# Kernel optimization log

Measured on AMD Instinct MI355X. Metric: run time of the kernel, lower is better.

The kernel has to match this reference:

```python
import jax, jax.numpy as jnp
import numpy as np

NUM_HEADS = 16
NUM_GROUPS = 4
HIDDEN = 2048
HEAD_DIM = HIDDEN // NUM_HEADS  # 128


def setup_inputs() -> dict:
    key = jax.random.key(0)
    ks = jax.random.split(key, 9)
    B, S = 2, 2048
    kv_dim = NUM_GROUPS * HEAD_DIM
    sc_in = 1.0 / np.sqrt(HIDDEN)
    return {
        "X": jax.random.normal(ks[0], (B, S, HIDDEN), dtype=jnp.float32),
        "Wq": jax.random.normal(ks[1], (HIDDEN, HIDDEN), dtype=jnp.float32) * sc_in,
        "bq": jnp.zeros((HIDDEN,), jnp.float32),
        "Wk": jax.random.normal(ks[2], (kv_dim, HIDDEN), dtype=jnp.float32) * sc_in,
        "bk": jnp.zeros((kv_dim,), jnp.float32),
        "Wv": jax.random.normal(ks[3], (kv_dim, HIDDEN), dtype=jnp.float32) * sc_in,
        "bv": jnp.zeros((kv_dim,), jnp.float32),
        "Wo": jax.random.normal(ks[4], (HIDDEN, HIDDEN), dtype=jnp.float32) * sc_in,
        "bo": jnp.zeros((HIDDEN,), jnp.float32),
    }


def reference(X, Wq, bq, Wk, bk, Wv, bv, Wo, bo):
    B, S, D = X.shape
    H, G, hd = NUM_HEADS, NUM_GROUPS, HEAD_DIM
    rep = H // G

    q = X @ Wq.T + bq                          # (B,S,D)
    k = X @ Wk.T + bk                          # (B,S,G*hd)
    v = X @ Wv.T + bv                          # (B,S,G*hd)

    q = q.reshape(B, S, H, hd).transpose(0, 2, 1, 3)   # (B,H,S,hd)
    k = k.reshape(B, S, G, hd).transpose(0, 2, 1, 3)   # (B,G,S,hd)
    v = v.reshape(B, S, G, hd).transpose(0, 2, 1, 3)
    # GQA head expansion: each kv group serves rep query heads
    k = jnp.repeat(k, rep, axis=1)             # (B,H,S,hd)
    v = jnp.repeat(v, rep, axis=1)

    scale = 1.0 / jnp.sqrt(jnp.asarray(hd, X.dtype))
    scores = jnp.einsum('bhqd,bhkd->bhqk', q, k) * scale  # (B,H,S,S)
    attn = jax.nn.softmax(scores, axis=-1)
    mid = jnp.einsum('bhqk,bhkd->bhqd', attn, v)          # (B,H,S,hd)
    mid = mid.transpose(0, 2, 1, 3).reshape(B, S, D)
    return mid @ Wo.T + bo
```

## Files before the change

kernel.cpp:

```cpp
#include <hip/hip_runtime.h>

using uint = unsigned int;
using ushort = unsigned short;

typedef float f32x4 __attribute__((ext_vector_type(4)));
typedef float f32x16 __attribute__((ext_vector_type(16)));
typedef uint u32x4 __attribute__((ext_vector_type(4)));
using short8 = __attribute__((ext_vector_type(8))) short;

__device__ __forceinline__ ushort f2bf(float f) {
  uint u = __float_as_uint(f);
  u += 0x7fffu + ((u >> 16) & 1u);
  return (ushort)(u >> 16);
}

#define GLOAD_LDS16(gptr, lptr)                                                   \
  __builtin_amdgcn_global_load_lds(                                               \
      (const __attribute__((address_space(1))) void*)(gptr),                      \
      (__attribute__((address_space(3))) void*)(lptr), 16, 0, 0)

__global__ void cast_all_bf16(const float* __restrict__ X,
                              const float* __restrict__ Wq,
                              const float* __restrict__ Wk,
                              const float* __restrict__ Wv,
                              const float* __restrict__ Wo,
                              ushort* __restrict__ dst ) {
  const int e0 = 2097152;
  const int e1 = e0 + 1048576;
  const int e2 = e1 + 262144;
  const int e3 = e2 + 262144;
  const int e4 = e3 + 1048576;
  const int stride = gridDim.x * blockDim.x;
  for (int i = blockIdx.x * blockDim.x + threadIdx.x; i < e4; i += stride) {
    const float* src;
    int j;
    if (i < e0)      { src = X;  j = i; }
    else if (i < e1) { src = Wq; j = i - e0; }
    else if (i < e2) { src = Wk; j = i - e1; }
    else if (i < e3) { src = Wv; j = i - e2; }
    else             { src = Wo; j = i - e3; }
    float4 v = reinterpret_cast<const float4*>(src)[j];
    ushort4 o;
    o.x = f2bf(v.x); o.y = f2bf(v.y); o.z = f2bf(v.z); o.w = f2bf(v.w);
    reinterpret_cast<ushort4*>(dst)[i] = o;
  }
}

__device__ __forceinline__ void gemm128_mainloop(const ushort* __restrict__ A,
                                                 const ushort* __restrict__ W,
                                                 int K, ushort* As, ushort* Bs,
                                                 f32x4 (&acc)[4][4]) {
  const int tid = threadIdx.x;
  const int lane = tid & 63;
  const int wr = (tid >> 7) & 1;
  const int wc = (tid >> 6) & 1;
  const char* aP = (const char*)(A + (size_t)(tid >> 2) * K) + (tid & 3) * 16;
  const char* bP = (const char*)(W + (size_t)(tid >> 2) * K) + (tid & 3) * 16;
  const size_t rowHop = (size_t)64 * K * 2;
  ushort* aL0 = As + tid * 8;
  ushort* aL1 = As + 2048 + tid * 8;
  ushort* bL0 = Bs + tid * 8;
  ushort* bL1 = Bs + 2048 + tid * 8;
  const int ar = lane & 15;
  const int ak = (lane >> 4) * 8;

  for (int k0 = 0; k0 < K; k0 += 32) {
    GLOAD_LDS16(aP, aL0);
    GLOAD_LDS16(aP + rowHop, aL1);
    GLOAD_LDS16(bP, bL0);
    GLOAD_LDS16(bP + rowHop, bL1);
    aP += 64; bP += 64;
    __syncthreads();
    short8 af[4], bf[4];
#pragma unroll
    for (int i = 0; i < 4; ++i)
      af[i] = *reinterpret_cast<const short8*>(&As[(wr * 64 + i * 16 + ar) * 32 + ak]);
#pragma unroll
    for (int i = 0; i < 4; ++i)
      bf[i] = *reinterpret_cast<const short8*>(&Bs[(wc * 64 + i * 16 + ar) * 32 + ak]);
#pragma unroll
    for (int mi = 0; mi < 4; ++mi)
#pragma unroll
      for (int ni = 0; ni < 4; ++ni)
        acc[mi][ni] = __builtin_amdgcn_mfma_f32_16x16x32_bf16(af[mi], bf[ni],
                                                              acc[mi][ni], 0, 0, 0);
    __syncthreads();
  }
}

__global__ __launch_bounds__(256) void qkv_gemm(
    const ushort* __restrict__ Xb, const ushort* __restrict__ Wq,
    const ushort* __restrict__ Wk, const ushort* __restrict__ Wv,
    const float* __restrict__ bq, const float* __restrict__ bk,
    const float* __restrict__ bv, ushort* __restrict__ Qb,
    ushort* __restrict__ Kb, ushort* __restrict__ Vf) {
  __shared__ ushort As[128 * 32], Bs[128 * 32];
  const int bx = blockIdx.x, by = blockIdx.y;
  const ushort* W; const float* bias; ushort* out;
  int n0, mode, ldo;
  if (bx < 16)      { W = Wq; bias = bq; out = Qb; n0 = bx * 128;        mode = 0; ldo = 2048; }
  else if (bx < 20) { W = Wk; bias = bk; out = Kb; n0 = (bx - 16) * 128; mode = 0; ldo = 512; }
  else              { W = Wv; bias = bv; out = Vf; n0 = (bx - 20) * 128; mode = 1; ldo = 0; }

  f32x4 acc[4][4] = {};
  gemm128_mainloop(Xb + (size_t)by * 128 * 2048, W + (size_t)n0 * 2048, 2048, As, Bs, acc);

  const int lane = threadIdx.x & 63;
  const int wr = (threadIdx.x >> 7) & 1, wc = (threadIdx.x >> 6) & 1;
  const int r0 = by * 128 + wr * 64 + ((lane >> 4) * 4);
  const int c0 = wc * 64 + (lane & 15);
#pragma unroll
  for (int mi = 0; mi < 4; ++mi)
#pragma unroll
    for (int ni = 0; ni < 4; ++ni) {
      const int col = c0 + ni * 16;
      const float bb = bias[n0 + col];
#pragma unroll
      for (int j = 0; j < 4; ++j) {
        const int row = r0 + mi * 16 + j;
        const float v = acc[mi][ni][j] + bb;
        if (mode == 0) {
          out[(size_t)row * ldo + n0 + col] = f2bf(v);
        } else {
          const int b2 = row >> 11, s = row & 2047;
          const int vc = n0 + col;
          const int g2 = vc >> 7, d = vc & 127;
          const int t2 = s >> 6, ks = (s >> 4) & 3, hi2 = (s >> 3) & 1, j2 = s & 7;
          const int dblk = d >> 5, lq2 = d & 31;
          out[(size_t)((b2 * 4 + g2) * 32 + t2) * 8192 +
              (ks * 4 + dblk) * 512 + (hi2 * 32 + lq2) * 8 + j2] = f2bf(v);
        }
      }
    }
}

__global__ __launch_bounds__(256) void out_gemm(const ushort* __restrict__ Mid,
                                                const ushort* __restrict__ Wo,
                                                const float* __restrict__ bo,
                                                float* __restrict__ Out) {
  __shared__ ushort As[128 * 32], Bs[128 * 32];
  const int bx = blockIdx.x, by = blockIdx.y;
  f32x4 acc[4][4] = {};
  gemm128_mainloop(Mid + (size_t)by * 128 * 2048, Wo + (size_t)bx * 128 * 2048,
                   2048, As, Bs, acc);
  const int lane = threadIdx.x & 63;
  const int wr = (threadIdx.x >> 7) & 1, wc = (threadIdx.x >> 6) & 1;
  const int r0 = by * 128 + wr * 64 + ((lane >> 4) * 4);
  const int c0 = bx * 128 + wc * 64 + (lane & 15);
#pragma unroll
  for (int mi = 0; mi < 4; ++mi)
#pragma unroll
    for (int ni = 0; ni < 4; ++ni) {
      const int col = c0 + ni * 16;
      const float bb = bo[col];
#pragma unroll
      for (int j = 0; j < 4; ++j)
        Out[(size_t)(r0 + mi * 16 + j) * 2048 + col] = acc[mi][ni][j] + bb;
    }
}

__global__ __launch_bounds__(256, 2) void attn_fwd(const ushort* __restrict__ Q,
                                                   const ushort* __restrict__ Kb,
                                                   const ushort* __restrict__ Vf,
                                                   ushort* __restrict__ Mid) {
  __shared__ ushort Ks[2][64 * 128];

  const int tid = threadIdx.x, lane = tid & 63, wave = tid >> 6;
  const int h = blockIdx.y, b = blockIdx.z, g = h >> 2;
  const int q0w = blockIdx.x * 128 + wave * 32;
  const int lq = lane & 31, hi = lane >> 5;

  const char* kbase = (const char*)Kb + ((size_t)b * 2048 * 512 + g * 128) * 2;
  int kRow[4], kOff[4];
#pragma unroll
  for (int i = 0; i < 4; ++i) {
    const int off = (i * 256 + tid) * 16;
    const int r = off >> 8, c = off & 255;
    kRow[i] = r; kOff[i] = c ^ ((r & 15) << 4);
  }

#pragma unroll
  for (int i = 0; i < 4; ++i)
    GLOAD_LDS16(kbase + (size_t)kRow[i] * 1024 + kOff[i],
                (char*)Ks[0] + (i * 256 + tid) * 16);

  const ushort* vfb = Vf + (size_t)(b * 4 + g) * 262144 + lane * 8;

  short8 qf[8];
  {
    const ushort* qp = Q + (size_t)(b * 2048 + q0w + lq) * 2048 + h * 128 + hi * 8;
#pragma unroll
    for (int dblk = 0; dblk < 8; ++dblk)
      qf[dblk] = *reinterpret_cast<const short8*>(qp + dblk * 16);
  }

  short8 onesf;
#pragma unroll
  for (int i = 0; i < 8; ++i) onesf[i] = (short)0x3F80;

  f32x16 o[4] = {};
  f32x16 ol = {};
  const float sc2 = 0.08838834764831843f * 1.44269504088896340736f;
  const float FM = 8.0f;

  __syncthreads();

  const int ksw = (lq & 15) << 4;

  for (int t = 0; t < 32; ++t) {
    const int cur = t & 1;

    short8 vr[16];
    {
      const ushort* vt = vfb + t * 8192;
#pragma unroll
      for (int u = 0; u < 16; ++u)
        vr[u] = *reinterpret_cast<const short8*>(vt + u * 512);
    }

    if (t < 31) {
      const int kv0 = (t + 1) * 64;
#pragma unroll
      for (int i = 0; i < 4; ++i)
        GLOAD_LDS16(kbase + (size_t)(kv0 + kRow[i]) * 1024 + kOff[i],
                    (char*)Ks[cur ^ 1] + (i * 256 + tid) * 16);
    }

    const char* ksb = (const char*)Ks[cur];
    f32x16 st0 = {}, st1 = {};
    __builtin_amdgcn_s_setprio(1);
#pragma unroll
    for (int dblk = 0; dblk < 8; ++dblk) {
      const int cb = (dblk * 32 + 16 * hi) ^ ksw;
      short8 kf0 = *reinterpret_cast<const short8*>(ksb + lq * 256 + cb);
      short8 kf1 = *reinterpret_cast<const short8*>(ksb + (32 + lq) * 256 + cb);
      st0 = __builtin_amdgcn_mfma_f32_32x32x16_bf16(kf0, qf[dblk], st0, 0, 0, 0);
      st1 = __builtin_amdgcn_mfma_f32_32x32x16_bf16(kf1, qf[dblk], st1, 0, 0, 0);
    }
    __builtin_amdgcn_s_setprio(0);

#pragma unroll
    for (int r = 0; r < 16; ++r) {
      st0[r] = exp2f(fmaf(st0[r], sc2, -FM));
      st1[r] = exp2f(fmaf(st1[r], sc2, -FM));
    }

    short8 pa[4];
#pragma unroll
    for (int half = 0; half < 2; ++half) {
      const f32x16 pt = half ? st1 : st0;
#pragma unroll
      for (int kk = 0; kk < 2; ++kk) {
        const int Rx = kk * 8;
        uint w0, w1, w2, w3;
#pragma unroll
        for (int s2 = 0; s2 < 2; ++s2) {
          const int s = s2 * 2;
          const float x0 = pt[Rx + s],     x1 = pt[Rx + s + 1];
          const float y0 = pt[Rx + 4 + s], y1 = pt[Rx + 4 + s + 1];
          uint x, y;
          asm("v_cvt_pk_bf16_f32 %0, %1, %2" : "=v"(x) : "v"(x0), "v"(x1));
          asm("v_cvt_pk_bf16_f32 %0, %1, %2" : "=v"(y) : "v"(y0), "v"(y1));
          auto sw = __builtin_amdgcn_permlane32_swap(x, y, false, false);
          if (s2 == 0) { w0 = sw[0]; w2 = sw[1]; }
          else         { w1 = sw[0]; w3 = sw[1]; }
        }
        u32x4 wv = {w0, w1, w2, w3};
        pa[half * 2 + kk] = __builtin_bit_cast(short8, wv);
      }
    }

    __builtin_amdgcn_s_setprio(1);
#pragma unroll
    for (int ks = 0; ks < 4; ++ks) {
#pragma unroll
      for (int dblk = 0; dblk < 4; ++dblk)
        o[dblk] = __builtin_amdgcn_mfma_f32_32x32x16_bf16(pa[ks], vr[ks * 4 + dblk],
                                                          o[dblk], 0, 0, 0);
      ol = __builtin_amdgcn_mfma_f32_32x32x16_bf16(pa[ks], onesf, ol, 0, 0, 0);
    }
    __builtin_amdgcn_s_setprio(0);

    __syncthreads();
  }

#pragma unroll
  for (int r = 0; r < 16; ++r) {
    const int qr = (r & 3) + 8 * (r >> 2) + 4 * hi;
    const float lv = 1.f / ol[r];
    ushort* mp = Mid + (size_t)(b * 2048 + q0w + qr) * 2048 + h * 128 + lq;
#pragma unroll
    for (int dblk = 0; dblk < 4; ++dblk)
      mp[dblk * 32] = f2bf(o[dblk][r] * lv);
  }
}

extern "C" void kernel_launch(void* const* d_in, const int* in_sizes, int n_in,
                              void* d_out, int out_size, void* d_ws, size_t ws_size,
                              hipStream_t stream) {
  const float* X  = (const float*)d_in[0];
  const float* Wq = (const float*)d_in[1];
  const float* bq = (const float*)d_in[2];
  const float* Wk = (const float*)d_in[3];
  const float* bk = (const float*)d_in[4];
  const float* Wv = (const float*)d_in[5];
  const float* bv = (const float*)d_in[6];
  const float* Wo = (const float*)d_in[7];
  const float* bo = (const float*)d_in[8];
  float* Out = (float*)d_out;

  char* ws = (char*)d_ws;
  ushort* Xb   = (ushort*)(ws);
  ushort* Wqb  = (ushort*)(ws + 16777216);
  ushort* Wkb  = (ushort*)(ws + 25165824);
  ushort* Wvb  = (ushort*)(ws + 27262976);
  ushort* Wob  = (ushort*)(ws + 29360128);
  ushort* Qb   = (ushort*)(ws + 37748736);
  ushort* Kbuf = (ushort*)(ws + 54525952);
  ushort* Vfb  = (ushort*)(ws + 58720256);
  ushort* Midb = (ushort*)(ws + 62914560);

  cast_all_bf16<<<dim3(2048), dim3(256), 0, stream>>>(X, Wq, Wk, Wv, Wo, Xb);

  qkv_gemm<<<dim3(24, 32), 256, 0, stream>>>(Xb, Wqb, Wkb, Wvb, bq, bk, bv,
                                             Qb, Kbuf, Vfb);
  attn_fwd<<<dim3(16, 16, 2), 256, 0, stream>>>(Qb, Kbuf, Vfb, Midb);
  out_gemm<<<dim3(16, 32), 256, 0, stream>>>(Midb, Wob, bo, Out);
}
```

Baseline: 218.9 us.

## Split attention KV range in two halves and merge partial outputs

Splits the attention key/value loop into two halves handled by separate blocks (grid z doubled), writing unnormalized bf16 partial outputs and row sums into reused workspace buffers. A new merge kernel adds the two partials and normalizes them into Mid. Launch bounds are raised to 4 blocks per CU. The goal is more parallelism and occupancy, since the original grid of 512 blocks underfills the GPU. In exchange it adds an extra kernel plus partial-output traffic, and rounds each partial to bf16 before the sum. The fixed softmax max offset is kept, so the two partials can be summed without rescaling.

```diff
diff --git a/kernel.cpp b/kernel.cpp
--- a/kernel.cpp
+++ b/kernel.cpp
@@ -12,6 +12,9 @@
   uint u = __float_as_uint(f);
   u += 0x7fffu + ((u >> 16) & 1u);
   return (ushort)(u >> 16);
+}
+__device__ __forceinline__ float bf2f(ushort v) {
+  return __uint_as_float(((uint)v) << 16);
 }
 
 #define GLOAD_LDS16(gptr, lptr)                                                   \
@@ -159,16 +162,21 @@
     }
 }
 
-__global__ __launch_bounds__(256, 2) void attn_fwd(const ushort* __restrict__ Q,
+__global__ __launch_bounds__(256, 4) void attn_fwd(const ushort* __restrict__ Q,
                                                    const ushort* __restrict__ Kb,
                                                    const ushort* __restrict__ Vf,
-                                                   ushort* __restrict__ Mid) {
+                                                   ushort* __restrict__ Op0,
+                                                   ushort* __restrict__ Op1,
+                                                   float* __restrict__ lp) {
   __shared__ ushort Ks[2][64 * 128];
 
   const int tid = threadIdx.x, lane = tid & 63, wave = tid >> 6;
-  const int h = blockIdx.y, b = blockIdx.z, g = h >> 2;
+  const int h = blockIdx.y;
+  const int half = blockIdx.z >> 1, b = blockIdx.z & 1;
+  const int g = h >> 2;
   const int q0w = blockIdx.x * 128 + wave * 32;
   const int lq = lane & 31, hi = lane >> 5;
+  const int t0 = half * 16, tEnd = t0 + 16;
 
   const char* kbase = (const char*)Kb + ((size_t)b * 2048 * 512 + g * 128) * 2;
   int kRow[4], kOff[4];
@@ -181,7 +189,7 @@
 
 #pragma unroll
   for (int i = 0; i < 4; ++i)
-    GLOAD_LDS16(kbase + (size_t)kRow[i] * 1024 + kOff[i],
+    GLOAD_LDS16(kbase + (size_t)(t0 * 64 + kRow[i]) * 1024 + kOff[i],
                 (char*)Ks[0] + (i * 256 + tid) * 16);
 
   const ushort* vfb = Vf + (size_t)(b * 4 + g) * 262144 + lane * 8;
@@ -207,7 +215,7 @@
 
   const int ksw = (lq & 15) << 4;
 
-  for (int t = 0; t < 32; ++t) {
+  for (int t = t0; t < tEnd; ++t) {
     const int cur = t & 1;
 
     short8 vr[16];
@@ -218,7 +226,7 @@
         vr[u] = *reinterpret_cast<const short8*>(vt + u * 512);
     }
 
-    if (t < 31) {
+    if (t + 1 < tEnd) {
       const int kv0 = (t + 1) * 64;
 #pragma unroll
       for (int i = 0; i < 4; ++i)
@@ -247,8 +255,8 @@
 
     short8 pa[4];
 #pragma unroll
-    for (int half = 0; half < 2; ++half) {
-      const f32x16 pt = half ? st1 : st0;
+    for (int halfp = 0; halfp < 2; ++halfp) {
+      const f32x16 pt = halfp ? st1 : st0;
 #pragma unroll
       for (int kk = 0; kk < 2; ++kk) {
         const int Rx = kk * 8;
@@ -266,7 +274,7 @@
           else         { w1 = sw[0]; w3 = sw[1]; }
         }
         u32x4 wv = {w0, w1, w2, w3};
-        pa[half * 2 + kk] = __builtin_bit_cast(short8, wv);
+        pa[halfp * 2 + kk] = __builtin_bit_cast(short8, wv);
       }
     }
 
@@ -284,14 +292,38 @@
     __syncthreads();
   }
 
+  ushort* opb = half ? Op1 : Op0;
 #pragma unroll
   for (int r = 0; r < 16; ++r) {
     const int qr = (r & 3) + 8 * (r >> 2) + 4 * hi;
-    const float lv = 1.f / ol[r];
-    ushort* mp = Mid + (size_t)(b * 2048 + q0w + qr) * 2048 + h * 128 + lq;
+    ushort* mp = opb + (size_t)(b * 2048 + q0w + qr) * 2048 + h * 128 + lq;
 #pragma unroll
     for (int dblk = 0; dblk < 4; ++dblk)
-      mp[dblk * 32] = f2bf(o[dblk][r] * lv);
+      mp[dblk * 32] = f2bf(o[dblk][r]);
+    if (lq == 0)
+      lp[((size_t)(half * 2 + b) * 2048 + q0w + qr) * 16 + h] = ol[r];
+  }
+}
+
+__global__ void attn_merge(const ushort* __restrict__ Op0,
+                           const ushort* __restrict__ Op1,
+                           const float* __restrict__ lp,
+                           ushort* __restrict__ Mid) {
+  const int N8 = (2 * 2048 * 2048) / 8;
+  const int stride = gridDim.x * blockDim.x;
+  for (int i = blockIdx.x * blockDim.x + threadIdx.x; i < N8; i += stride) {
+    const int e = i * 8;
+    const int b = e >> 22, q = (e >> 11) & 2047, h = (e >> 7) & 15;
+    const float l0 = lp[((size_t)b * 2048 + q) * 16 + h];
+    const float l1 = lp[((size_t)(2 + b) * 2048 + q) * 16 + h];
+    const float inv = 1.f / (l0 + l1);
+    short8 a = reinterpret_cast<const short8*>(Op0)[i];
+    short8 c = reinterpret_cast<const short8*>(Op1)[i];
+    short8 out;
+#pragma unroll
+    for (int j = 0; j < 8; ++j)
+      out[j] = (short)f2bf((bf2f((ushort)a[j]) + bf2f((ushort)c[j])) * inv);
+    reinterpret_cast<short8*>(Mid)[i] = out;
   }
 }
 
@@ -319,11 +351,15 @@
   ushort* Kbuf = (ushort*)(ws + 54525952);
   ushort* Vfb  = (ushort*)(ws + 58720256);
   ushort* Midb = (ushort*)(ws + 62914560);
+  ushort* Op0  = Xb;
+  ushort* Op1  = (ushort*)(ws + 79691776);
+  float*  lpb  = (float*)Wqb;
 
   cast_all_bf16<<<dim3(2048), dim3(256), 0, stream>>>(X, Wq, Wk, Wv, Wo, Xb);
 
   qkv_gemm<<<dim3(24, 32), 256, 0, stream>>>(Xb, Wqb, Wkb, Wvb, bq, bk, bv,
                                              Qb, Kbuf, Vfb);
-  attn_fwd<<<dim3(16, 16, 2), 256, 0, stream>>>(Qb, Kbuf, Vfb, Midb);
+  attn_fwd<<<dim3(16, 16, 4), 256, 0, stream>>>(Qb, Kbuf, Vfb, Op0, Op1, lpb);
+  attn_merge<<<dim3(2048), dim3(256), 0, stream>>>(Op0, Op1, lpb, Midb);
   out_gemm<<<dim3(16, 32), 256, 0, stream>>>(Midb, Wob, bo, Out);
 }
```

New measurement: 656.3 us. +199.8%, slower.

## Split attention KV range across two wave groups and merge partial results

Applied to the files above, without the earlier changes.

The attention block grows to 512 threads. Two groups of four waves each process half of the KV sequence (16 tiles each) for the same 128 queries, each group with its own double-buffered K staging in LDS. The partial outputs and row sums are merged through shared memory at the end. The V register loads are also split into two halves so the second half is issued after the QK MFMAs, which shortens register live ranges. The partial O from the second group is stored as bf16 before the merge, which adds a small rounding error, and LDS use rises to 64KB per block.

```diff
diff --git a/kernel.cpp b/kernel.cpp
--- a/kernel.cpp
+++ b/kernel.cpp
@@ -12,6 +12,9 @@
   uint u = __float_as_uint(f);
   u += 0x7fffu + ((u >> 16) & 1u);
   return (ushort)(u >> 16);
+}
+__device__ __forceinline__ float bf2f(ushort v) {
+  return __uint_as_float(((uint)v) << 16);
 }
 
 #define GLOAD_LDS16(gptr, lptr)                                                   \
@@ -159,30 +162,35 @@
     }
 }
 
-__global__ __launch_bounds__(256, 2) void attn_fwd(const ushort* __restrict__ Q,
-                                                   const ushort* __restrict__ Kb,
-                                                   const ushort* __restrict__ Vf,
-                                                   ushort* __restrict__ Mid) {
-  __shared__ ushort Ks[2][64 * 128];
+__global__ __launch_bounds__(512) void attn_fwd(const ushort* __restrict__ Q,
+                                                const ushort* __restrict__ Kb,
+                                                const ushort* __restrict__ Vf,
+                                                ushort* __restrict__ Mid) {
+  __shared__ char shm[65536];
 
   const int tid = threadIdx.x, lane = tid & 63, wave = tid >> 6;
   const int h = blockIdx.y, b = blockIdx.z, g = h >> 2;
-  const int q0w = blockIdx.x * 128 + wave * 32;
+  const int half = wave >> 2, wsub = wave & 3;
+  const int q0w = blockIdx.x * 128 + wsub * 32;
   const int lq = lane & 31, hi = lane >> 5;
-
+  const int t0 = half * 16;
+
+  const int sstream = tid >> 8;
+  const int ltid = tid & 255;
+  char* sbase = shm + sstream * 32768;
   const char* kbase = (const char*)Kb + ((size_t)b * 2048 * 512 + g * 128) * 2;
   int kRow[4], kOff[4];
 #pragma unroll
   for (int i = 0; i < 4; ++i) {
-    const int off = (i * 256 + tid) * 16;
+    const int off = (i * 256 + ltid) * 16;
     const int r = off >> 8, c = off & 255;
     kRow[i] = r; kOff[i] = c ^ ((r & 15) << 4);
   }
 
 #pragma unroll
   for (int i = 0; i < 4; ++i)
-    GLOAD_LDS16(kbase + (size_t)kRow[i] * 1024 + kOff[i],
-                (char*)Ks[0] + (i * 256 + tid) * 16);
+    GLOAD_LDS16(kbase + (size_t)(sstream * 1024 + kRow[i]) * 1024 + kOff[i],
+                sbase + (i * 256 + ltid) * 16);
 
   const ushort* vfb = Vf + (size_t)(b * 4 + g) * 262144 + lane * 8;
 
@@ -206,27 +214,29 @@
   __syncthreads();
 
   const int ksw = (lq & 15) << 4;
-
-  for (int t = 0; t < 32; ++t) {
+  const char* kwave = shm + half * 32768;
+
+  for (int t = 0; t < 16; ++t) {
     const int cur = t & 1;
-
-    short8 vr[16];
+    const int gt = t0 + t;
+
+    short8 vrA[8], vrB[8];
     {
-      const ushort* vt = vfb + t * 8192;
-#pragma unroll
-      for (int u = 0; u < 16; ++u)
-        vr[u] = *reinterpret_cast<const short8*>(vt + u * 512);
-    }
-
-    if (t < 31) {
-      const int kv0 = (t + 1) * 64;
+      const ushort* vt = vfb + gt * 8192;
+#pragma unroll
+      for (int u = 0; u < 8; ++u)
+        vrA[u] = *reinterpret_cast<const short8*>(vt + u * 512);
+    }
+
+    if (t < 15) {
+      const int kv0 = (sstream * 16 + t + 1) * 64;
 #pragma unroll
       for (int i = 0; i < 4; ++i)
         GLOAD_LDS16(kbase + (size_t)(kv0 + kRow[i]) * 1024 + kOff[i],
-                    (char*)Ks[cur ^ 1] + (i * 256 + tid) * 16);
-    }
-
-    const char* ksb = (const char*)Ks[cur];
+                    sbase + (cur ^ 1) * 16384 + (i * 256 + ltid) * 16);
+    }
+
+    const char* ksb = kwave + cur * 16384;
     f32x16 st0 = {}, st1 = {};
     __builtin_amdgcn_s_setprio(1);
 #pragma unroll
@@ -239,6 +249,13 @@
     }
     __builtin_amdgcn_s_setprio(0);
 
+    {
+      const ushort* vt = vfb + gt * 8192;
+#pragma unroll
+      for (int u = 0; u < 8; ++u)
+        vrB[u] = *reinterpret_cast<const short8*>(vt + (8 + u) * 512);
+    }
+
 #pragma unroll
     for (int r = 0; r < 16; ++r) {
       st0[r] = exp2f(fmaf(st0[r], sc2, -FM));
@@ -247,8 +264,8 @@
 
     short8 pa[4];
 #pragma unroll
-    for (int half = 0; half < 2; ++half) {
-      const f32x16 pt = half ? st1 : st0;
+    for (int halfp = 0; halfp < 2; ++halfp) {
+      const f32x16 pt = halfp ? st1 : st0;
 #pragma unroll
       for (int kk = 0; kk < 2; ++kk) {
         const int Rx = kk * 8;
@@ -266,32 +283,58 @@
           else         { w1 = sw[0]; w3 = sw[1]; }
         }
         u32x4 wv = {w0, w1, w2, w3};
-        pa[half * 2 + kk] = __builtin_bit_cast(short8, wv);
+        pa[halfp * 2 + kk] = __builtin_bit_cast(short8, wv);
       }
     }
 
     __builtin_amdgcn_s_setprio(1);
 #pragma unroll
-    for (int ks = 0; ks < 4; ++ks) {
+    for (int ks = 0; ks < 2; ++ks) {
 #pragma unroll
       for (int dblk = 0; dblk < 4; ++dblk)
-        o[dblk] = __builtin_amdgcn_mfma_f32_32x32x16_bf16(pa[ks], vr[ks * 4 + dblk],
+        o[dblk] = __builtin_amdgcn_mfma_f32_32x32x16_bf16(pa[ks], vrA[ks * 4 + dblk],
                                                           o[dblk], 0, 0, 0);
       ol = __builtin_amdgcn_mfma_f32_32x32x16_bf16(pa[ks], onesf, ol, 0, 0, 0);
     }
+#pragma unroll
+    for (int ks = 2; ks < 4; ++ks) {
+#pragma unroll
+      for (int dblk = 0; dblk < 4; ++dblk)
+        o[dblk] = __builtin_amdgcn_mfma_f32_32x32x16_bf16(pa[ks], vrB[(ks - 2) * 4 + dblk],
+                                                          o[dblk], 0, 0, 0);
+      ol = __builtin_amdgcn_mfma_f32_32x32x16_bf16(pa[ks], onesf, ol, 0, 0, 0);
+    }
     __builtin_amdgcn_s_setprio(0);
 
     __syncthreads();
   }
 
-#pragma unroll
-  for (int r = 0; r < 16; ++r) {
-    const int qr = (r & 3) + 8 * (r >> 2) + 4 * hi;
-    const float lv = 1.f / ol[r];
-    ushort* mp = Mid + (size_t)(b * 2048 + q0w + qr) * 2048 + h * 128 + lq;
+  ushort* ob = (ushort*)shm;
+  float*  lb = (float*)(shm + 32768);
+  if (half == 1) {
 #pragma unroll
     for (int dblk = 0; dblk < 4; ++dblk)
-      mp[dblk * 32] = f2bf(o[dblk][r] * lv);
+#pragma unroll
+      for (int r = 0; r < 16; ++r)
+        ob[wsub * 4096 + (dblk * 16 + r) * 64 + lane] = f2bf(o[dblk][r]);
+#pragma unroll
+    for (int r = 0; r < 16; ++r)
+      lb[wsub * 1024 + r * 64 + lane] = ol[r];
+  }
+  __syncthreads();
+
+  if (half == 0) {
+#pragma unroll
+    for (int r = 0; r < 16; ++r) {
+      const int qr = (r & 3) + 8 * (r >> 2) + 4 * hi;
+      const float lv = 1.f / (ol[r] + lb[wsub * 1024 + r * 64 + lane]);
+      ushort* mp = Mid + (size_t)(b * 2048 + q0w + qr) * 2048 + h * 128 + lq;
+#pragma unroll
+      for (int dblk = 0; dblk < 4; ++dblk) {
+        const float v = o[dblk][r] + bf2f(ob[wsub * 4096 + (dblk * 16 + r) * 64 + lane]);
+        mp[dblk * 32] = f2bf(v * lv);
+      }
+    }
   }
 }
 
@@ -324,6 +367,6 @@
 
   qkv_gemm<<<dim3(24, 32), 256, 0, stream>>>(Xb, Wqb, Wkb, Wvb, bq, bk, bv,
                                              Qb, Kbuf, Vfb);
-  attn_fwd<<<dim3(16, 16, 2), 256, 0, stream>>>(Qb, Kbuf, Vfb, Midb);
+  attn_fwd<<<dim3(16, 16, 2), 512, 0, stream>>>(Qb, Kbuf, Vfb, Midb);
   out_gemm<<<dim3(16, 32), 256, 0, stream>>>(Midb, Wob, bo, Out);
 }
```

After: 226.8 us. 3.6% more time.

## Switch attention to 16x16x32 MFMA with 16-row query tiles per wave

Applied to the files above, without the earlier changes.

Rewrites the attention kernel to use 16x16x32 bf16 MFMAs, with each wave owning 16 query rows instead of 32, and doubles the grid to 32 query blocks. The V fragment layout written by the QKV GEMM epilogue is changed to match the new MFMA operand layout, which removes the permlane32 swaps when packing P. V loads are split into four staged chunks interleaved with the PV MFMAs to lower register pressure, and the occupancy hint in launch_bounds is dropped. In exchange, each K tile in LDS is reused by half as many query rows, so the same K/V traffic is spread over twice as many blocks.

```diff
diff --git a/kernel.cpp b/kernel.cpp
--- a/kernel.cpp
+++ b/kernel.cpp
@@ -4,7 +4,6 @@
 using ushort = unsigned short;
 
 typedef float f32x4 __attribute__((ext_vector_type(4)));
-typedef float f32x16 __attribute__((ext_vector_type(16)));
 typedef uint u32x4 __attribute__((ext_vector_type(4)));
 using short8 = __attribute__((ext_vector_type(8))) short;
 
@@ -125,10 +124,15 @@
           const int b2 = row >> 11, s = row & 2047;
           const int vc = n0 + col;
           const int g2 = vc >> 7, d = vc & 127;
-          const int t2 = s >> 6, ks = (s >> 4) & 3, hi2 = (s >> 3) & 1, j2 = s & 7;
-          const int dblk = d >> 5, lq2 = d & 31;
+          const int t2 = s >> 6;
+          const int ks = (s >> 5) & 1;
+          const int jhi = (s >> 4) & 1;
+          const int gp2 = (s >> 2) & 3;
+          const int j2 = jhi * 4 + (s & 3);
+          const int dt = d >> 4, dl = d & 15;
+          const int l = gp2 * 16 + dl;
           out[(size_t)((b2 * 4 + g2) * 32 + t2) * 8192 +
-              (ks * 4 + dblk) * 512 + (hi2 * 32 + lq2) * 8 + j2] = f2bf(v);
+              (ks * 8 + dt) * 512 + l * 8 + j2] = f2bf(v);
         }
       }
     }
@@ -159,16 +163,16 @@
     }
 }
 
-__global__ __launch_bounds__(256, 2) void attn_fwd(const ushort* __restrict__ Q,
-                                                   const ushort* __restrict__ Kb,
-                                                   const ushort* __restrict__ Vf,
-                                                   ushort* __restrict__ Mid) {
+__global__ __launch_bounds__(256) void attn_fwd(const ushort* __restrict__ Q,
+                                                const ushort* __restrict__ Kb,
+                                                const ushort* __restrict__ Vf,
+                                                ushort* __restrict__ Mid) {
   __shared__ ushort Ks[2][64 * 128];
 
   const int tid = threadIdx.x, lane = tid & 63, wave = tid >> 6;
   const int h = blockIdx.y, b = blockIdx.z, g = h >> 2;
-  const int q0w = blockIdx.x * 128 + wave * 32;
-  const int lq = lane & 31, hi = lane >> 5;
+  const int q0w = blockIdx.x * 64 + wave * 16;
+  const int lq = lane & 15, gp = lane >> 4;
 
   const char* kbase = (const char*)Kb + ((size_t)b * 2048 * 512 + g * 128) * 2;
   int kRow[4], kOff[4];
@@ -186,37 +190,38 @@
 
   const ushort* vfb = Vf + (size_t)(b * 4 + g) * 262144 + lane * 8;
 
-  short8 qf[8];
+  short8 qf[4];
   {
-    const ushort* qp = Q + (size_t)(b * 2048 + q0w + lq) * 2048 + h * 128 + hi * 8;
-#pragma unroll
-    for (int dblk = 0; dblk < 8; ++dblk)
-      qf[dblk] = *reinterpret_cast<const short8*>(qp + dblk * 16);
+    const ushort* qp = Q + (size_t)(b * 2048 + q0w + lq) * 2048 + h * 128 + gp * 8;
+#pragma unroll
+    for (int c = 0; c < 4; ++c)
+      qf[c] = *reinterpret_cast<const short8*>(qp + c * 32);
   }
 
   short8 onesf;
 #pragma unroll
   for (int i = 0; i < 8; ++i) onesf[i] = (short)0x3F80;
 
-  f32x16 o[4] = {};
-  f32x16 ol = {};
+  f32x4 o[8] = {};
+  f32x4 ol = {};
   const float sc2 = 0.08838834764831843f * 1.44269504088896340736f;
   const float FM = 8.0f;
 
   __syncthreads();
 
-  const int ksw = (lq & 15) << 4;
+  const int ksw = lq << 4;
 
   for (int t = 0; t < 32; ++t) {
     const int cur = t & 1;
-
-    short8 vr[16];
-    {
-      const ushort* vt = vfb + t * 8192;
-#pragma unroll
-      for (int u = 0; u < 16; ++u)
-        vr[u] = *reinterpret_cast<const short8*>(vt + u * 512);
-    }
+    const ushort* vt = vfb + t * 8192;
+
+    short8 vrA0[4], vrA1[4];
+#pragma unroll
+    for (int u = 0; u < 4; ++u)
+      vrA0[u] = *reinterpret_cast<const short8*>(vt + u * 512);
+#pragma unroll
+    for (int u = 0; u < 4; ++u)
+      vrA1[u] = *reinterpret_cast<const short8*>(vt + (4 + u) * 512);
 
     if (t < 31) {
       const int kv0 = (t + 1) * 64;
@@ -227,71 +232,83 @@
     }
 
     const char* ksb = (const char*)Ks[cur];
-    f32x16 st0 = {}, st1 = {};
+    f32x4 st[4] = {};
     __builtin_amdgcn_s_setprio(1);
 #pragma unroll
-    for (int dblk = 0; dblk < 8; ++dblk) {
-      const int cb = (dblk * 32 + 16 * hi) ^ ksw;
-      short8 kf0 = *reinterpret_cast<const short8*>(ksb + lq * 256 + cb);
-      short8 kf1 = *reinterpret_cast<const short8*>(ksb + (32 + lq) * 256 + cb);
-      st0 = __builtin_amdgcn_mfma_f32_32x32x16_bf16(kf0, qf[dblk], st0, 0, 0, 0);
-      st1 = __builtin_amdgcn_mfma_f32_32x32x16_bf16(kf1, qf[dblk], st1, 0, 0, 0);
+    for (int c = 0; c < 4; ++c) {
+      const int cb = (c * 64 + gp * 16) ^ ksw;
+#pragma unroll
+      for (int kvt = 0; kvt < 4; ++kvt) {
+        short8 kf = *reinterpret_cast<const short8*>(ksb + (kvt * 16 + lq) * 256 + cb);
+        st[kvt] = __builtin_amdgcn_mfma_f32_16x16x32_bf16(kf, qf[c], st[kvt], 0, 0, 0);
+      }
     }
     __builtin_amdgcn_s_setprio(0);
 
 #pragma unroll
-    for (int r = 0; r < 16; ++r) {
-      st0[r] = exp2f(fmaf(st0[r], sc2, -FM));
-      st1[r] = exp2f(fmaf(st1[r], sc2, -FM));
-    }
-
-    short8 pa[4];
-#pragma unroll
-    for (int half = 0; half < 2; ++half) {
-      const f32x16 pt = half ? st1 : st0;
-#pragma unroll
-      for (int kk = 0; kk < 2; ++kk) {
-        const int Rx = kk * 8;
-        uint w0, w1, w2, w3;
-#pragma unroll
-        for (int s2 = 0; s2 < 2; ++s2) {
-          const int s = s2 * 2;
-          const float x0 = pt[Rx + s],     x1 = pt[Rx + s + 1];
-          const float y0 = pt[Rx + 4 + s], y1 = pt[Rx + 4 + s + 1];
-          uint x, y;
-          asm("v_cvt_pk_bf16_f32 %0, %1, %2" : "=v"(x) : "v"(x0), "v"(x1));
-          asm("v_cvt_pk_bf16_f32 %0, %1, %2" : "=v"(y) : "v"(y0), "v"(y1));
-          auto sw = __builtin_amdgcn_permlane32_swap(x, y, false, false);
-          if (s2 == 0) { w0 = sw[0]; w2 = sw[1]; }
-          else         { w1 = sw[0]; w3 = sw[1]; }
-        }
-        u32x4 wv = {w0, w1, w2, w3};
-        pa[half * 2 + kk] = __builtin_bit_cast(short8, wv);
-      }
+    for (int kvt = 0; kvt < 4; ++kvt)
+#pragma unroll
+      for (int r = 0; r < 4; ++r)
+        st[kvt][r] = exp2f(fmaf(st[kvt][r], sc2, -FM));
+
+    uint w[4][2];
+#pragma unroll
+    for (int kvt = 0; kvt < 4; ++kvt) {
+      asm("v_cvt_pk_bf16_f32 %0, %1, %2" : "=v"(w[kvt][0]) : "v"(st[kvt][0]), "v"(st[kvt][1]));
+      asm("v_cvt_pk_bf16_f32 %0, %1, %2" : "=v"(w[kvt][1]) : "v"(st[kvt][2]), "v"(st[kvt][3]));
+    }
+    short8 pa[2];
+    {
+      u32x4 wv0 = {w[0][0], w[0][1], w[1][0], w[1][1]};
+      u32x4 wv1 = {w[2][0], w[2][1], w[3][0], w[3][1]};
+      pa[0] = __builtin_bit_cast(short8, wv0);
+      pa[1] = __builtin_bit_cast(short8, wv1);
     }
 
     __builtin_amdgcn_s_setprio(1);
 #pragma unroll
-    for (int ks = 0; ks < 4; ++ks) {
-#pragma unroll
-      for (int dblk = 0; dblk < 4; ++dblk)
-        o[dblk] = __builtin_amdgcn_mfma_f32_32x32x16_bf16(pa[ks], vr[ks * 4 + dblk],
-                                                          o[dblk], 0, 0, 0);
-      ol = __builtin_amdgcn_mfma_f32_32x32x16_bf16(pa[ks], onesf, ol, 0, 0, 0);
-    }
+    for (int dt = 0; dt < 4; ++dt)
+      o[dt] = __builtin_amdgcn_mfma_f32_16x16x32_bf16(pa[0], vrA0[dt], o[dt], 0, 0, 0);
+    ol = __builtin_amdgcn_mfma_f32_16x16x32_bf16(pa[0], onesf, ol, 0, 0, 0);
     __builtin_amdgcn_s_setprio(0);
 
+    short8 vrB0[4];
+#pragma unroll
+    for (int u = 0; u < 4; ++u)
+      vrB0[u] = *reinterpret_cast<const short8*>(vt + (8 + u) * 512);
+
+    __builtin_amdgcn_s_setprio(1);
+#pragma unroll
+    for (int dt = 0; dt < 4; ++dt)
+      o[4 + dt] = __builtin_amdgcn_mfma_f32_16x16x32_bf16(pa[0], vrA1[dt], o[4 + dt], 0, 0, 0);
+    __builtin_amdgcn_s_setprio(0);
+
+    short8 vrB1[4];
+#pragma unroll
+    for (int u = 0; u < 4; ++u)
+      vrB1[u] = *reinterpret_cast<const short8*>(vt + (12 + u) * 512);
+
+    __builtin_amdgcn_s_setprio(1);
+#pragma unroll
+    for (int dt = 0; dt < 4; ++dt)
+      o[dt] = __builtin_amdgcn_mfma_f32_16x16x32_bf16(pa[1], vrB0[dt], o[dt], 0, 0, 0);
+    ol = __builtin_amdgcn_mfma_f32_16x16x32_bf16(pa[1], onesf, ol, 0, 0, 0);
+#pragma unroll
+    for (int dt = 0; dt < 4; ++dt)
+      o[4 + dt] = __builtin_amdgcn_mfma_f32_16x16x32_bf16(pa[1], vrB1[dt], o[4 + dt], 0, 0, 0);
+    __builtin_amdgcn_s_setprio(0);
+
     __syncthreads();
   }
 
 #pragma unroll
-  for (int r = 0; r < 16; ++r) {
-    const int qr = (r & 3) + 8 * (r >> 2) + 4 * hi;
+  for (int r = 0; r < 4; ++r) {
+    const int q = q0w + gp * 4 + r;
     const float lv = 1.f / ol[r];
-    ushort* mp = Mid + (size_t)(b * 2048 + q0w + qr) * 2048 + h * 128 + lq;
-#pragma unroll
-    for (int dblk = 0; dblk < 4; ++dblk)
-      mp[dblk * 32] = f2bf(o[dblk][r] * lv);
+    ushort* mp = Mid + (size_t)(b * 2048 + q) * 2048 + h * 128 + lq;
+#pragma unroll
+    for (int dt = 0; dt < 8; ++dt)
+      mp[dt * 16] = f2bf(o[dt][r] * lv);
   }
 }
 
@@ -324,6 +341,6 @@
 
   qkv_gemm<<<dim3(24, 32), 256, 0, stream>>>(Xb, Wqb, Wkb, Wvb, bq, bk, bv,
                                              Qb, Kbuf, Vfb);
-  attn_fwd<<<dim3(16, 16, 2), 256, 0, stream>>>(Qb, Kbuf, Vfb, Midb);
+  attn_fwd<<<dim3(32, 16, 2), 256, 0, stream>>>(Qb, Kbuf, Vfb, Midb);
   out_gemm<<<dim3(16, 32), 256, 0, stream>>>(Midb, Wob, bo, Out);
 }
```

Result: slower. 243.5 us (+11.3%).
